# Kernel optimization log

Measured on AMD Instinct MI355X. Metric: run time of the kernel, lower is better.

## Reference

```python
import jax, jax.numpy as jnp
import numpy as np

B, S, H, NH = 2, 2048, 2048, 16
HD = H // NH


def setup_inputs() -> dict:
    key = jax.random.key(0)
    ks = jax.random.split(key, 10)
    s = 1.0 / np.sqrt(H)
    x = jax.random.normal(ks[0], (B, S, H), dtype=jnp.float32)
    # additive causal mask: 0 on/below diagonal, -1e9 above
    causal = jnp.tril(jnp.ones((S, S), dtype=bool))
    mask = jnp.where(causal, 0.0, -1e9).astype(jnp.float32)[None, None]
    return {
        "x": x,
        "mask": mask,
        "wq": jax.random.normal(ks[1], (H, H), jnp.float32) * s,
        "bq": jnp.zeros((H,), jnp.float32),
        "wk": jax.random.normal(ks[2], (H, H), jnp.float32) * s,
        "bk": jnp.zeros((H,), jnp.float32),
        "wv": jax.random.normal(ks[3], (H, H), jnp.float32) * s,
        "bv": jnp.zeros((H,), jnp.float32),
        "wo": jax.random.normal(ks[4], (H, H), jnp.float32) * s,
        "bo": jnp.zeros((H,), jnp.float32),
    }


def reference(x, mask, wq, bq, wk, bk, wv, bv, wo, bo):
    b, s, _ = x.shape
    scale = HD ** (-0.5)
    # projections -> [b, nh, s, hd]
    def split_heads(t):
        return t.reshape(b, s, NH, HD).transpose(0, 2, 1, 3)
    q = split_heads(x @ wq + bq)
    k = split_heads(x @ wk + bk)
    v = split_heads(x @ wv + bv)
    scores = jnp.einsum('bhqd,bhkd->bhqk', q, k) * scale + mask
    attn = jax.nn.softmax(scores, axis=-1)
    out = jnp.einsum('bhqk,bhkd->bhqd', attn, v)
    out = out.transpose(0, 2, 1, 3).reshape(b, s, H)
    return out @ wo + bo
```

## Files before the change

kernel.cpp:

```cpp
#include <hip/hip_runtime.h>


using bf16x8 = __attribute__((ext_vector_type(8))) short;
using bf16x4 = __attribute__((ext_vector_type(4))) short;
using f32x4  = __attribute__((ext_vector_type(4))) float;

#define S_LEN 2048
#define NHEAD 16
#define HDIM  128
#define HID   2048

__device__ __forceinline__ unsigned short f2bf(float f) {
    unsigned int u = __float_as_uint(f);
    u += 0x7fffu + ((u >> 16) & 1u);
    return (unsigned short)(u >> 16);
}
__device__ __forceinline__ void gl2lds16(const void* g, void* l) {
    __builtin_amdgcn_global_load_lds(
        (const __attribute__((address_space(1))) void*)g,
        (__attribute__((address_space(3))) void*)l, 16, 0, 0);
}

__device__ __forceinline__ f32x4 pv_mfma(bf16x4 a, bf16x4 b, f32x4 c) {
#if defined(__HIP_DEVICE_COMPILE__)
#if __has_builtin(__builtin_amdgcn_mfma_f32_16x16x16bf16_1k)
    return __builtin_amdgcn_mfma_f32_16x16x16bf16_1k(a, b, c, 0, 0, 0);
#else
    asm("v_mfma_f32_16x16x16_bf16 %0, %1, %2, %0" : "+v"(c) : "v"(a), "v"(b));
    return c;
#endif
#else
    (void)a; (void)b;
    return c;
#endif
}

__global__ void convert_x(const float* __restrict__ x, unsigned short* __restrict__ xb) {
    int i = (blockIdx.x * 256 + threadIdx.x) * 4;
    float4 v = *(const float4*)(x + i);
    ushort4 o;
    o.x = f2bf(v.x); o.y = f2bf(v.y); o.z = f2bf(v.z); o.w = f2bf(v.w);
    *(ushort4*)(xb + i) = o;
}

__global__ void convert_wt(const float* __restrict__ w0, const float* __restrict__ w1,
                           const float* __restrict__ w2, const float* __restrict__ w3,
                           unsigned short* __restrict__ t0, unsigned short* __restrict__ t1,
                           unsigned short* __restrict__ t2, unsigned short* __restrict__ t3) {
    __shared__ float tile[64][65];
    int z = blockIdx.z;
    const float* src = (z == 0) ? w0 : (z == 1) ? w1 : (z == 2) ? w2 : w3;
    unsigned short* dst = (z == 0) ? t0 : (z == 1) ? t1 : (z == 2) ? t2 : t3;
    int r0 = blockIdx.y * 64, c0 = blockIdx.x * 64;
    int t = threadIdx.x;
    for (int i = t; i < 64 * 64; i += 256) {
        int r = i >> 6, c = i & 63;
        tile[r][c] = src[(size_t)(r0 + r) * HID + c0 + c];
    }
    __syncthreads();
    for (int i = t; i < 64 * 64; i += 256) {
        int r = i & 63, c = i >> 6;
        dst[(size_t)(c0 + c) * HID + r0 + r] = f2bf(tile[r][c]);
    }
}

template <int MODE>
__launch_bounds__(256, 2)
__global__ void gemm_bt(const unsigned short* __restrict__ A,
                        const unsigned short* __restrict__ Bt0,
                        const unsigned short* __restrict__ Bt1,
                        const unsigned short* __restrict__ Bt2,
                        const float* __restrict__ bias0,
                        const float* __restrict__ bias1,
                        const float* __restrict__ bias2,
                        unsigned short* __restrict__ C0,
                        unsigned short* __restrict__ C1,
                        unsigned short* __restrict__ C2,
                        float* __restrict__ Cf) {
    __shared__ __align__(16) unsigned short As[128 * 32];
    __shared__ __align__(16) unsigned short Bs[128 * 32];

    const unsigned short* Bt = Bt0;
    const float* bias = bias0;
    unsigned short* C = C0;
    if (MODE == 1) {
        int z = blockIdx.z;
        if (z == 1) { Bt = Bt1; bias = bias1; C = C1; }
        else if (z == 2) { Bt = Bt2; bias = bias2; C = C2; }
    }

    const int K = HID;
    int m0 = blockIdx.y * 128;
    int n0 = blockIdx.x * 128;
    int tid = threadIdx.x;
    int lane = tid & 63;
    int w = tid >> 6;
    int wr = w >> 1, wc = w & 1;
    int l15 = lane & 15;
    int quad = lane >> 4;

    f32x4 acc[4][4];
#pragma unroll
    for (int i = 0; i < 4; ++i)
#pragma unroll
        for (int j = 0; j < 4; ++j) acc[i][j] = (f32x4){0.f, 0.f, 0.f, 0.f};

    int srow = w * 16 + (lane >> 2);
    int scol = (lane & 3) * 8;
    const unsigned short* gA = A + (size_t)(m0 + srow) * K + scol;
    const unsigned short* gB = Bt + (size_t)(n0 + srow) * K + scol;
    unsigned short* lA = &As[w * 512];
    unsigned short* lB = &Bs[w * 512];

    for (int k0 = 0; k0 < K; k0 += 32) {
        gl2lds16(gA + k0,                  lA);
        gl2lds16(gA + (size_t)64 * K + k0, lA + 2048);
        gl2lds16(gB + k0,                  lB);
        gl2lds16(gB + (size_t)64 * K + k0, lB + 2048);
        __syncthreads();

        bf16x8 av[4], bv[4];
        int q8 = quad * 8;
#pragma unroll
        for (int i = 0; i < 4; ++i) av[i] = *(const bf16x8*)&As[(wr * 64 + i * 16 + l15) * 32 + q8];
#pragma unroll
        for (int j = 0; j < 4; ++j) bv[j] = *(const bf16x8*)&Bs[(wc * 64 + j * 16 + l15) * 32 + q8];
#pragma unroll
        for (int i = 0; i < 4; ++i)
#pragma unroll
            for (int j = 0; j < 4; ++j)
                acc[i][j] = __builtin_amdgcn_mfma_f32_16x16x32_bf16(av[i], bv[j], acc[i][j], 0, 0, 0);
        __syncthreads();
    }

    int zz = (MODE == 1) ? blockIdx.z : 0;
#pragma unroll
    for (int j = 0; j < 4; ++j) {
        int n = n0 + wc * 64 + j * 16 + l15;
        float bn = bias[n];
#pragma unroll
        for (int i = 0; i < 4; ++i) {
            int mb = m0 + wr * 64 + i * 16 + quad * 4;
            if (MODE == 1 && zz == 2) {
                int b = mb >> 11, s = mb & 2047, h = n >> 7, d = n & 127;
                int kt = s >> 4, qv = (s >> 2) & 3, ct = d >> 4, lv = d & 15;
                size_t addr = ((((size_t)((b << 4) + h) * 128 + kt) * 4 + (ct >> 1)) * 4 + qv) * 128
                              + lv * 8 + (ct & 1) * 4;
                ushort4 o;
                o.x = f2bf(acc[i][j][0] + bn);
                o.y = f2bf(acc[i][j][1] + bn);
                o.z = f2bf(acc[i][j][2] + bn);
                o.w = f2bf(acc[i][j][3] + bn);
                *(ushort4*)&C[addr] = o;
            } else {
#pragma unroll
                for (int reg = 0; reg < 4; ++reg) {
                    int m = mb + reg;
                    float v = acc[i][j][reg] + bn;
                    if (MODE == 0) {
                        Cf[(size_t)m * HID + n] = v;
                    } else {
                        int b = m >> 11, s = m & 2047, h = n >> 7, d = n & 127;
                        if (zz == 1) {
                            int kt = s >> 4, lk = s & 15, kk = d >> 5, qk = (d >> 3) & 3, e = d & 7;
                            size_t addr = ((((size_t)((b << 4) + h) * 128 + kt) * 4 + kk) * 4 + qk) * 128
                                          + lk * 8 + e;
                            C[addr] = f2bf(v);
                        } else {
                            C[(size_t)(((b << 4) + h) * S_LEN + s) * HDIM + d] = f2bf(v);
                        }
                    }
                }
            }
        }
    }
}

__launch_bounds__(256, 4)
__global__ void attn_kernel(const unsigned short* __restrict__ Qg,
                            const unsigned short* __restrict__ Kp,
                            const unsigned short* __restrict__ Vp,
                            unsigned short* __restrict__ O) {
    int linear = blockIdx.y * 32 + blockIdx.x;
    int xcd = linear & 7;
    int u = linear >> 3;
    int bh = xcd * 4 + (u & 3);
    int j = u >> 2;
    int b = bh >> 4, h = bh & 15;

    int tid = threadIdx.x, lane = tid & 63, w = tid >> 6;
    int l15 = lane & 15, quad = lane >> 4;

    int role = (w + (u >> 5)) & 3;
    int strip = (role < 2) ? (2 * j + role) : (126 - 2 * j + (role - 2));
    int r0 = strip * 16;

    const unsigned short* Qb = Qg + (size_t)bh * (S_LEN * HDIM);
    const unsigned short* Kb = Kp + (size_t)bh * 262144 + quad * 128 + l15 * 8;
    const unsigned short* Vb = Vp + (size_t)bh * 262144 + quad * 128 + l15 * 8;

    bf16x8 qf[4];
#pragma unroll
    for (int kk = 0; kk < 4; ++kk)
        qf[kk] = *(const bf16x8*)&Qb[(size_t)(r0 + l15) * HDIM + kk * 32 + quad * 8];

    f32x4 o_acc[8];
#pragma unroll
    for (int c = 0; c < 8; ++c) o_acc[c] = (f32x4){0.f, 0.f, 0.f, 0.f};
    float l_part = 0.f;

    const float k2 = 0.08838834764831845f * 1.4426950408889634f;

    int nkt = strip + 1;

    bf16x8 kA[4], kB[4], v[4];

#define LOADK(dst, t) do { size_t _o = (size_t)(t) * 2048;                         \
    dst[0] = *(const bf16x8*)&Kb[_o];                                              \
    dst[1] = *(const bf16x8*)&Kb[_o + 512];                                        \
    dst[2] = *(const bf16x8*)&Kb[_o + 1024];                                       \
    dst[3] = *(const bf16x8*)&Kb[_o + 1536]; } while (0)

#define LOADV(dst, t) do { size_t _o = (size_t)(t) * 2048;                         \
    dst[0] = *(const bf16x8*)&Vb[_o];                                              \
    dst[1] = *(const bf16x8*)&Vb[_o + 512];                                        \
    dst[2] = *(const bf16x8*)&Vb[_o + 1024];                                       \
    dst[3] = *(const bf16x8*)&Vb[_o + 1536]; } while (0)

#define VLO(x) __builtin_shufflevector(x, x, 0, 1, 2, 3)
#define VHI(x) __builtin_shufflevector(x, x, 4, 5, 6, 7)

#define TILE(kreg, t) do {                                                         \
    f32x4 st0 = (f32x4){0.f, 0.f, 0.f, 0.f};                                       \
    f32x4 st1 = (f32x4){0.f, 0.f, 0.f, 0.f};                                       \
    st0 = __builtin_amdgcn_mfma_f32_16x16x32_bf16(kreg[0], qf[0], st0, 0, 0, 0);   \
    st1 = __builtin_amdgcn_mfma_f32_16x16x32_bf16(kreg[1], qf[1], st1, 0, 0, 0);   \
    st0 = __builtin_amdgcn_mfma_f32_16x16x32_bf16(kreg[2], qf[2], st0, 0, 0, 0);   \
    st1 = __builtin_amdgcn_mfma_f32_16x16x32_bf16(kreg[3], qf[3], st1, 0, 0, 0);   \
    f32x4 stv = st0 + st1;                                                         \
    float p0, p1, p2, p3;                                                          \
    if ((t) == nkt - 1) {                                                          \
        p0 = (quad * 4 + 0 <= l15) ? exp2f(stv[0] * k2) : 0.f;                     \
        p1 = (quad * 4 + 1 <= l15) ? exp2f(stv[1] * k2) : 0.f;                     \
        p2 = (quad * 4 + 2 <= l15) ? exp2f(stv[2] * k2) : 0.f;                     \
        p3 = (quad * 4 + 3 <= l15) ? exp2f(stv[3] * k2) : 0.f;                     \
    } else {                                                                       \
        p0 = exp2f(stv[0] * k2); p1 = exp2f(stv[1] * k2);                          \
        p2 = exp2f(stv[2] * k2); p3 = exp2f(stv[3] * k2);                          \
    }                                                                              \
    l_part += (p0 + p1) + (p2 + p3);                                               \
    bf16x4 pf;                                                                     \
    pf[0] = (short)f2bf(p0); pf[1] = (short)f2bf(p1);                              \
    pf[2] = (short)f2bf(p2); pf[3] = (short)f2bf(p3);                              \
    o_acc[0] = pv_mfma(pf, VLO(v[0]), o_acc[0]);                                   \
    o_acc[1] = pv_mfma(pf, VHI(v[0]), o_acc[1]);                                   \
    o_acc[2] = pv_mfma(pf, VLO(v[1]), o_acc[2]);                                   \
    o_acc[3] = pv_mfma(pf, VHI(v[1]), o_acc[3]);                                   \
    o_acc[4] = pv_mfma(pf, VLO(v[2]), o_acc[4]);                                   \
    o_acc[5] = pv_mfma(pf, VHI(v[2]), o_acc[5]);                                   \
    o_acc[6] = pv_mfma(pf, VLO(v[3]), o_acc[6]);                                   \
    o_acc[7] = pv_mfma(pf, VHI(v[3]), o_acc[7]);                                   \
} while (0)

    LOADK(kA, 0);
    int kt = 0;
    while (true) {
        int ktn = (kt + 1 < nkt) ? kt + 1 : kt;
        LOADV(v, kt);
        LOADK(kB, ktn);
        TILE(kA, kt);
        if (++kt >= nkt) break;

        ktn = (kt + 1 < nkt) ? kt + 1 : kt;
        LOADV(v, kt);
        LOADK(kA, ktn);
        TILE(kB, kt);
        if (++kt >= nkt) break;
    }

#undef TILE
#undef LOADK
#undef LOADV
#undef VLO
#undef VHI

    l_part += __shfl_xor(l_part, 16, 64);
    l_part += __shfl_xor(l_part, 32, 64);

#pragma unroll
    for (int reg = 0; reg < 4; ++reg) {
        float l = __shfl(l_part, quad * 4 + reg, 64);
        float inv = 1.f / l;
        int srow = r0 + quad * 4 + reg;
        unsigned short* op = O + (size_t)(b * S_LEN + srow) * HID + h * HDIM;
#pragma unroll
        for (int ct = 0; ct < 8; ++ct)
            op[ct * 16 + l15] = f2bf(o_acc[ct][reg] * inv);
    }
}

extern "C" void kernel_launch(void* const* d_in, const int* in_sizes, int n_in,
                              void* d_out, int out_size, void* d_ws, size_t ws_size,
                              hipStream_t stream) {
    (void)in_sizes; (void)n_in; (void)out_size; (void)ws_size;
    const float* x  = (const float*)d_in[0];
    const float* wq = (const float*)d_in[2];
    const float* bq = (const float*)d_in[3];
    const float* wk = (const float*)d_in[4];
    const float* bk = (const float*)d_in[5];
    const float* wv = (const float*)d_in[6];
    const float* bv = (const float*)d_in[7];
    const float* wo = (const float*)d_in[8];
    const float* bo = (const float*)d_in[9];
    float* out = (float*)d_out;

    unsigned short* ws = (unsigned short*)d_ws;
    const size_t WSZ = 4194304;
    unsigned short* wqT = ws;
    unsigned short* wkT = ws + WSZ;
    unsigned short* wvT = ws + 2 * WSZ;
    unsigned short* woT = ws + 3 * WSZ;
    unsigned short* xb  = ws + 4 * WSZ;
    unsigned short* Ab  = ws + 4 * WSZ;
    unsigned short* Qb  = ws + 6 * WSZ;
    unsigned short* Kb  = ws + 8 * WSZ;
    unsigned short* Vb  = ws + 10 * WSZ;

    convert_x<<<dim3(8192), 256, 0, stream>>>(x, xb);
    convert_wt<<<dim3(32, 32, 4), 256, 0, stream>>>(wq, wk, wv, wo, wqT, wkT, wvT, woT);
    gemm_bt<1><<<dim3(16, 32, 3), 256, 0, stream>>>(xb, wqT, wkT, wvT, bq, bk, bv,
                                                    Qb, Kb, Vb, nullptr);
    attn_kernel<<<dim3(32, 32), 256, 0, stream>>>(Qb, Kb, Vb, Ab);
    gemm_bt<0><<<dim3(16, 32, 1), 256, 0, stream>>>(Ab, woT, nullptr, nullptr,
                                                    bo, nullptr, nullptr,
                                                    nullptr, nullptr, nullptr, out);
}
```

Measured before the change: 424.9 us.

## Rewrite projection GEMMs as 8-wave double-buffered 128x256 tiles with swizzled LDS

Replaces the single-buffered 128x128, 4-wave GEMM with a 512-thread kernel that computes 128x256 tiles over a K=64 step. It double-buffers LDS so global-to-LDS loads overlap MFMA work, using explicit vmcnt/lgkmcnt waits, barriers and setprio. It also XOR-swizzles the LDS layout to avoid bank conflicts and remaps the 1D grid so blocks sharing a weight panel are spread across XCDs. The aim is to hide memory latency and raise MFMA utilisation in the QKV and output projections, at the cost of more LDS (96KB) and hand-tuned synchronisation that is fragile to get right.

```diff
diff --git a/kernel.cpp b/kernel.cpp
--- a/kernel.cpp
+++ b/kernel.cpp
@@ -65,39 +65,56 @@
 }
 
 template <int MODE>
-__launch_bounds__(256, 2)
-__global__ void gemm_bt(const unsigned short* __restrict__ A,
-                        const unsigned short* __restrict__ Bt0,
-                        const unsigned short* __restrict__ Bt1,
-                        const unsigned short* __restrict__ Bt2,
-                        const float* __restrict__ bias0,
-                        const float* __restrict__ bias1,
-                        const float* __restrict__ bias2,
-                        unsigned short* __restrict__ C0,
-                        unsigned short* __restrict__ C1,
-                        unsigned short* __restrict__ C2,
-                        float* __restrict__ Cf) {
-    __shared__ __align__(16) unsigned short As[128 * 32];
-    __shared__ __align__(16) unsigned short Bs[128 * 32];
+__launch_bounds__(512, 2)
+__global__ void gemm8(const unsigned short* __restrict__ A,
+                      const unsigned short* __restrict__ Bt0,
+                      const unsigned short* __restrict__ Bt1,
+                      const unsigned short* __restrict__ Bt2,
+                      const float* __restrict__ bias0,
+                      const float* __restrict__ bias1,
+                      const float* __restrict__ bias2,
+                      unsigned short* __restrict__ C0,
+                      unsigned short* __restrict__ C1,
+                      unsigned short* __restrict__ C2,
+                      float* __restrict__ Cf) {
+    __shared__ __align__(16) unsigned short lds[49152];
+    unsigned short* const A0 = lds;
+    unsigned short* const A1 = lds + 8192;
+    unsigned short* const B0 = lds + 16384;
+    unsigned short* const B1 = lds + 32768;
+
+    const int CPX = (MODE == 1) ? 96 : 32;
+    int vb = (blockIdx.x & 7) * CPX + (blockIdx.x >> 3);
+    int m0  = (vb & 31) * 128;
+    int n0g = (vb >> 5) * 256;
 
     const unsigned short* Bt = Bt0;
     const float* bias = bias0;
     unsigned short* C = C0;
+    int z = 0;
     if (MODE == 1) {
-        int z = blockIdx.z;
+        z = n0g >> 11;
         if (z == 1) { Bt = Bt1; bias = bias1; C = C1; }
         else if (z == 2) { Bt = Bt2; bias = bias2; C = C2; }
     }
-
-    const int K = HID;
-    int m0 = blockIdx.y * 128;
-    int n0 = blockIdx.x * 128;
+    int nb0 = n0g & 2047;
+
     int tid = threadIdx.x;
     int lane = tid & 63;
-    int w = tid >> 6;
-    int wr = w >> 1, wc = w & 1;
-    int l15 = lane & 15;
-    int quad = lane >> 4;
+    int wv_ = tid >> 6;
+    int wr = wv_ >> 2, wc = wv_ & 3;
+    int l15 = lane & 15, quad = lane >> 4;
+
+    int tr = tid >> 3;
+    int tc = ((tid & 7) ^ (tr & 7)) << 3;
+    const unsigned short* gA = A  + (size_t)(m0  + tr) * HID + tc;
+    const unsigned short* gB = Bt + (size_t)(nb0 + tr) * HID + tc;
+    const int td8 = tid * 8;
+
+    int arow = (wr * 64 + l15) * 64;
+    int brow = (wc * 64 + l15) * 64;
+    int sw0 = ((quad ^ (l15 & 7)) << 3);
+    int sw1 = (((4 + quad) ^ (l15 & 7)) << 3);
 
     f32x4 acc[4][4];
 #pragma unroll
@@ -105,43 +122,93 @@
 #pragma unroll
         for (int j = 0; j < 4; ++j) acc[i][j] = (f32x4){0.f, 0.f, 0.f, 0.f};
 
-    int srow = w * 16 + (lane >> 2);
-    int scol = (lane & 3) * 8;
-    const unsigned short* gA = A + (size_t)(m0 + srow) * K + scol;
-    const unsigned short* gB = Bt + (size_t)(n0 + srow) * K + scol;
-    unsigned short* lA = &As[w * 512];
-    unsigned short* lB = &Bs[w * 512];
-
-    for (int k0 = 0; k0 < K; k0 += 32) {
-        gl2lds16(gA + k0,                  lA);
-        gl2lds16(gA + (size_t)64 * K + k0, lA + 2048);
-        gl2lds16(gB + k0,                  lB);
-        gl2lds16(gB + (size_t)64 * K + k0, lB + 2048);
-        __syncthreads();
-
-        bf16x8 av[4], bv[4];
-        int q8 = quad * 8;
-#pragma unroll
-        for (int i = 0; i < 4; ++i) av[i] = *(const bf16x8*)&As[(wr * 64 + i * 16 + l15) * 32 + q8];
-#pragma unroll
-        for (int j = 0; j < 4; ++j) bv[j] = *(const bf16x8*)&Bs[(wc * 64 + j * 16 + l15) * 32 + q8];
-#pragma unroll
-        for (int i = 0; i < 4; ++i)
-#pragma unroll
-            for (int j = 0; j < 4; ++j)
-                acc[i][j] = __builtin_amdgcn_mfma_f32_16x16x32_bf16(av[i], bv[j], acc[i][j], 0, 0, 0);
-        __syncthreads();
-    }
-
-    int zz = (MODE == 1) ? blockIdx.z : 0;
+#define STAGE8(kt, AD, BD) do { int _kc = (kt) * 64;                        \
+    gl2lds16(gA + _kc,              (AD) + td8);                            \
+    gl2lds16(gA + 64 * HID + _kc,   (AD) + 4096 + td8);                     \
+    gl2lds16(gB + _kc,              (BD) + td8);                            \
+    gl2lds16(gB + 64 * HID + _kc,   (BD) + 4096 + td8);                     \
+    gl2lds16(gB + 128 * HID + _kc,  (BD) + 8192 + td8);                     \
+    gl2lds16(gB + 192 * HID + _kc,  (BD) + 12288 + td8); } while (0)
+
+#define FENCE() asm volatile("" ::: "memory")
+#define BAR()   do { FENCE(); __builtin_amdgcn_s_barrier(); FENCE(); } while (0)
+#define WAIT_LGKM0() do { asm volatile("s_waitcnt lgkmcnt(0)" ::: "memory");      \
+                          __builtin_amdgcn_sched_barrier(0); } while (0)
+#define WAIT_VM6()   do { asm volatile("s_waitcnt vmcnt(6)" ::: "memory");        \
+                          __builtin_amdgcn_sched_barrier(0); } while (0)
+
+    auto ktile = [&](unsigned short* AD, unsigned short* BD, int ks) {
+        {
+            bf16x8 av[4], bv[4];
+            av[0] = *(const bf16x8*)(AD + arow + sw0);
+            av[1] = *(const bf16x8*)(AD + arow + 1024 + sw0);
+            av[2] = *(const bf16x8*)(AD + arow + 2048 + sw0);
+            av[3] = *(const bf16x8*)(AD + arow + 3072 + sw0);
+            bv[0] = *(const bf16x8*)(BD + brow + sw0);
+            bv[1] = *(const bf16x8*)(BD + brow + 1024 + sw0);
+            bv[2] = *(const bf16x8*)(BD + brow + 2048 + sw0);
+            bv[3] = *(const bf16x8*)(BD + brow + 3072 + sw0);
+            BAR();
+            WAIT_LGKM0();
+            __builtin_amdgcn_s_setprio(1);
+#pragma unroll
+            for (int mi = 0; mi < 4; ++mi)
+#pragma unroll
+                for (int jj = 0; jj < 4; ++jj)
+                    acc[mi][jj] = __builtin_amdgcn_mfma_f32_16x16x32_bf16(av[mi], bv[jj], acc[mi][jj], 0, 0, 0);
+            __builtin_amdgcn_s_setprio(0);
+            BAR();
+        }
+        {
+            bf16x8 av[4], bv[4];
+            av[0] = *(const bf16x8*)(AD + arow + sw1);
+            av[1] = *(const bf16x8*)(AD + arow + 1024 + sw1);
+            av[2] = *(const bf16x8*)(AD + arow + 2048 + sw1);
+            av[3] = *(const bf16x8*)(AD + arow + 3072 + sw1);
+            bv[0] = *(const bf16x8*)(BD + brow + sw1);
+            bv[1] = *(const bf16x8*)(BD + brow + 1024 + sw1);
+            bv[2] = *(const bf16x8*)(BD + brow + 2048 + sw1);
+            bv[3] = *(const bf16x8*)(BD + brow + 3072 + sw1);
+            WAIT_LGKM0();
+            BAR();
+            STAGE8(ks, AD, BD);
+            __builtin_amdgcn_s_setprio(1);
+#pragma unroll
+            for (int mi = 0; mi < 4; ++mi)
+#pragma unroll
+                for (int jj = 0; jj < 4; ++jj)
+                    acc[mi][jj] = __builtin_amdgcn_mfma_f32_16x16x32_bf16(av[mi], bv[jj], acc[mi][jj], 0, 0, 0);
+            __builtin_amdgcn_s_setprio(0);
+            WAIT_VM6();
+            BAR();
+        }
+    };
+
+    STAGE8(0, A0, B0);
+    STAGE8(1, A1, B1);
+    WAIT_VM6();
+    BAR();
+
+    for (int t = 0; t < 32; t += 2) {
+        ktile(A0, B0, (t + 2 < 32) ? t + 2 : 31);
+        ktile(A1, B1, (t + 3 < 32) ? t + 3 : 31);
+    }
+    asm volatile("s_waitcnt vmcnt(0)" ::: "memory");
+
+#undef STAGE8
+#undef FENCE
+#undef BAR
+#undef WAIT_LGKM0
+#undef WAIT_VM6
+
 #pragma unroll
     for (int j = 0; j < 4; ++j) {
-        int n = n0 + wc * 64 + j * 16 + l15;
+        int n = nb0 + wc * 64 + j * 16 + l15;
         float bn = bias[n];
 #pragma unroll
         for (int i = 0; i < 4; ++i) {
             int mb = m0 + wr * 64 + i * 16 + quad * 4;
-            if (MODE == 1 && zz == 2) {
+            if (MODE == 1 && z == 2) {
                 int b = mb >> 11, s = mb & 2047, h = n >> 7, d = n & 127;
                 int kt = s >> 4, qv = (s >> 2) & 3, ct = d >> 4, lv = d & 15;
                 size_t addr = ((((size_t)((b << 4) + h) * 128 + kt) * 4 + (ct >> 1)) * 4 + qv) * 128
@@ -161,7 +228,7 @@
                         Cf[(size_t)m * HID + n] = v;
                     } else {
                         int b = m >> 11, s = m & 2047, h = n >> 7, d = n & 127;
-                        if (zz == 1) {
+                        if (z == 1) {
                             int kt = s >> 4, lk = s & 15, kk = d >> 5, qk = (d >> 3) & 3, e = d & 7;
                             size_t addr = ((((size_t)((b << 4) + h) * 128 + kt) * 4 + kk) * 4 + qk) * 128
                                           + lk * 8 + e;
@@ -328,10 +395,10 @@
 
     convert_x<<<dim3(8192), 256, 0, stream>>>(x, xb);
     convert_wt<<<dim3(32, 32, 4), 256, 0, stream>>>(wq, wk, wv, wo, wqT, wkT, wvT, woT);
-    gemm_bt<1><<<dim3(16, 32, 3), 256, 0, stream>>>(xb, wqT, wkT, wvT, bq, bk, bv,
-                                                    Qb, Kb, Vb, nullptr);
+    gemm8<1><<<dim3(768), 512, 0, stream>>>(xb, wqT, wkT, wvT, bq, bk, bv,
+                                            Qb, Kb, Vb, nullptr);
     attn_kernel<<<dim3(32, 32), 256, 0, stream>>>(Qb, Kb, Vb, Ab);
-    gemm_bt<0><<<dim3(16, 32, 1), 256, 0, stream>>>(Ab, woT, nullptr, nullptr,
-                                                    bo, nullptr, nullptr,
-                                                    nullptr, nullptr, nullptr, out);
-}
+    gemm8<0><<<dim3(256), 512, 0, stream>>>(Ab, woT, nullptr, nullptr,
+                                            bo, nullptr, nullptr,
+                                            nullptr, nullptr, nullptr, out);
+}
```

Result: faster. 408.9 us (-3.8%).

## Rewrite projection GEMMs as 256x256 double-buffered swizzled MFMA kernel

Applied to the files above, without the earlier changes.

Replaces the 128x128 single-buffered GEMM with a 256x256-tile, 512-thread kernel that uses a K-step of 64. Global-to-LDS loads are double-buffered and interleaved with MFMA work through explicit waitcnt and sched barriers, and the kernel raises wave priority around the MFMA blocks. LDS addresses are XOR-swizzled to avoid bank conflicts, and block IDs are remapped across XCDs. The aim is more data reuse per tile and load latency hidden behind compute. In exchange it uses 128KB of LDS and many more registers per block, and leaves fewer blocks in the grid (128 for the output projection), which may underfill the CUs.

```diff
diff --git a/kernel.cpp b/kernel.cpp
--- a/kernel.cpp
+++ b/kernel.cpp
@@ -65,8 +65,8 @@
 }
 
 template <int MODE>
-__launch_bounds__(256, 2)
-__global__ void gemm_bt(const unsigned short* __restrict__ A,
+__launch_bounds__(512, 2)
+__global__ void gemm256(const unsigned short* __restrict__ A,
                         const unsigned short* __restrict__ Bt0,
                         const unsigned short* __restrict__ Bt1,
                         const unsigned short* __restrict__ Bt2,
@@ -77,71 +77,146 @@
                         unsigned short* __restrict__ C1,
                         unsigned short* __restrict__ C2,
                         float* __restrict__ Cf) {
-    __shared__ __align__(16) unsigned short As[128 * 32];
-    __shared__ __align__(16) unsigned short Bs[128 * 32];
+    __shared__ __align__(16) unsigned short lds[65536];
+    unsigned short* const A0 = lds;
+    unsigned short* const A1 = lds + 16384;
+    unsigned short* const B0 = lds + 32768;
+    unsigned short* const B1 = lds + 49152;
+
+    const int CPX = (MODE == 1) ? 48 : 16;
+    int vb = (blockIdx.x & 7) * CPX + (blockIdx.x >> 3);
+    int m0  = (vb & 15) * 256;
+    int n0g = (vb >> 4) * 256;
 
     const unsigned short* Bt = Bt0;
     const float* bias = bias0;
     unsigned short* C = C0;
+    int z = 0;
     if (MODE == 1) {
-        int z = blockIdx.z;
+        z = n0g >> 11;
         if (z == 1) { Bt = Bt1; bias = bias1; C = C1; }
         else if (z == 2) { Bt = Bt2; bias = bias2; C = C2; }
     }
-
-    const int K = HID;
-    int m0 = blockIdx.y * 128;
-    int n0 = blockIdx.x * 128;
+    int nb0 = n0g & 2047;
+
     int tid = threadIdx.x;
     int lane = tid & 63;
-    int w = tid >> 6;
-    int wr = w >> 1, wc = w & 1;
-    int l15 = lane & 15;
-    int quad = lane >> 4;
-
-    f32x4 acc[4][4];
-#pragma unroll
-    for (int i = 0; i < 4; ++i)
+    int wv_ = tid >> 6;
+    int wr = wv_ >> 2, wc = wv_ & 3;
+    int l15 = lane & 15, quad = lane >> 4;
+
+    int tr = tid >> 3;
+    int tc = ((tid & 7) ^ (tr & 7)) << 3;
+    const unsigned short* gA = A  + (size_t)(m0  + tr) * HID + tc;
+    const unsigned short* gB = Bt + (size_t)(nb0 + tr) * HID + tc;
+    const int td8 = tid * 8;
+
+    int arow0 = (wr * 128 + l15) * 64;
+    int brow0 = (wc * 64 + l15) * 64;
+    int sw0 = ((quad ^ (l15 & 7)) << 3);
+    int sw1 = (((4 + quad) ^ (l15 & 7)) << 3);
+
+    f32x4 acc[8][4];
+#pragma unroll
+    for (int i = 0; i < 8; ++i)
 #pragma unroll
         for (int j = 0; j < 4; ++j) acc[i][j] = (f32x4){0.f, 0.f, 0.f, 0.f};
 
-    int srow = w * 16 + (lane >> 2);
-    int scol = (lane & 3) * 8;
-    const unsigned short* gA = A + (size_t)(m0 + srow) * K + scol;
-    const unsigned short* gB = Bt + (size_t)(n0 + srow) * K + scol;
-    unsigned short* lA = &As[w * 512];
-    unsigned short* lB = &Bs[w * 512];
-
-    for (int k0 = 0; k0 < K; k0 += 32) {
-        gl2lds16(gA + k0,                  lA);
-        gl2lds16(gA + (size_t)64 * K + k0, lA + 2048);
-        gl2lds16(gB + k0,                  lB);
-        gl2lds16(gB + (size_t)64 * K + k0, lB + 2048);
-        __syncthreads();
-
-        bf16x8 av[4], bv[4];
-        int q8 = quad * 8;
-#pragma unroll
-        for (int i = 0; i < 4; ++i) av[i] = *(const bf16x8*)&As[(wr * 64 + i * 16 + l15) * 32 + q8];
-#pragma unroll
-        for (int j = 0; j < 4; ++j) bv[j] = *(const bf16x8*)&Bs[(wc * 64 + j * 16 + l15) * 32 + q8];
-#pragma unroll
-        for (int i = 0; i < 4; ++i)
-#pragma unroll
-            for (int j = 0; j < 4; ++j)
-                acc[i][j] = __builtin_amdgcn_mfma_f32_16x16x32_bf16(av[i], bv[j], acc[i][j], 0, 0, 0);
-        __syncthreads();
-    }
-
-    int zz = (MODE == 1) ? blockIdx.z : 0;
+    bf16x8 aX[4], aY[4], b0v[4], b1v[4];
+
+#define STAGE(kt, AD, BD) do { int _kc = (kt) * 64;                          \
+    gl2lds16(gA + _kc,             (AD) + td8);                              \
+    gl2lds16(gA + 64 * HID + _kc,  (AD) + 4096 + td8);                       \
+    gl2lds16(gA + 128 * HID + _kc, (AD) + 8192 + td8);                       \
+    gl2lds16(gA + 192 * HID + _kc, (AD) + 12288 + td8);                      \
+    gl2lds16(gB + _kc,             (BD) + td8);                              \
+    gl2lds16(gB + 64 * HID + _kc,  (BD) + 4096 + td8);                       \
+    gl2lds16(gB + 128 * HID + _kc, (BD) + 8192 + td8);                       \
+    gl2lds16(gB + 192 * HID + _kc, (BD) + 12288 + td8); } while (0)
+
+#define LDA4(dst, AD, QB, SW) do {                                           \
+    dst[0] = *(const bf16x8*)((AD) + arow0 + ((QB) + 0) * 1024 + (SW));      \
+    dst[1] = *(const bf16x8*)((AD) + arow0 + ((QB) + 1) * 1024 + (SW));      \
+    dst[2] = *(const bf16x8*)((AD) + arow0 + ((QB) + 2) * 1024 + (SW));      \
+    dst[3] = *(const bf16x8*)((AD) + arow0 + ((QB) + 3) * 1024 + (SW)); } while (0)
+
+#define LDB4(dst, BD, SW) do {                                               \
+    dst[0] = *(const bf16x8*)((BD) + brow0 + 0 * 1024 + (SW));               \
+    dst[1] = *(const bf16x8*)((BD) + brow0 + 1 * 1024 + (SW));               \
+    dst[2] = *(const bf16x8*)((BD) + brow0 + 2 * 1024 + (SW));               \
+    dst[3] = *(const bf16x8*)((BD) + brow0 + 3 * 1024 + (SW)); } while (0)
+
+#define MF16(Q, a, b) do {                                                   \
+    __builtin_amdgcn_s_setprio(1);                                           \
+    _Pragma("unroll")                                                        \
+    for (int mi = 0; mi < 4; ++mi)                                           \
+        _Pragma("unroll")                                                    \
+        for (int nj = 0; nj < 4; ++nj)                                       \
+            acc[(Q) * 4 + mi][nj] =                                          \
+                __builtin_amdgcn_mfma_f32_16x16x32_bf16(a[mi], b[nj],        \
+                                                        acc[(Q) * 4 + mi][nj], 0, 0, 0); \
+    __builtin_amdgcn_s_setprio(0); } while (0)
+
+#define SCHED0() __builtin_amdgcn_sched_barrier(0)
+#define BAR()    do { asm volatile("" ::: "memory");                         \
+                      __builtin_amdgcn_s_barrier();                          \
+                      asm volatile("" ::: "memory"); } while (0)
+#define W_LGKM(N) do { asm volatile("s_waitcnt lgkmcnt(" #N ")" ::: "memory"); SCHED0(); } while (0)
+#define W_VM8()   do { asm volatile("s_waitcnt vmcnt(8)" ::: "memory");        SCHED0(); } while (0)
+
+#define TILE4(AD, BD, AN, BN_, ks) do {                                      \
+    LDA4(aY, AD, 4, sw0);                         \
+    W_LGKM(4);                                             \
+    MF16(0, aX, b0v);                                                        \
+    LDA4(aX, AD, 0, sw1);                                                    \
+    LDB4(b1v, BD, sw1);                                \
+    W_LGKM(8);                                                 \
+    MF16(1, aY, b0v);                                                        \
+    LDA4(aY, AD, 4, sw1);                         \
+    W_LGKM(4);                                             \
+    MF16(0, aX, b1v);                                                        \
+    W_LGKM(0);                       \
+    BAR();                               \
+    STAGE(ks, AD, BD);                           \
+    W_VM8();                              \
+    BAR();                                   \
+    LDA4(aX, AN, 0, sw0);                                                    \
+    LDB4(b0v, BN_, sw0);                   \
+    SCHED0();                                                                \
+    MF16(1, aY, b1v);                        \
+} while (0)
+
+    STAGE(0, A0, B0);
+    STAGE(1, A1, B1);
+    W_VM8();
+    BAR();
+    LDA4(aX, A0, 0, sw0);
+    LDB4(b0v, B0, sw0);
+
+    for (int t = 0; t < 32; t += 2) {
+        TILE4(A0, B0, A1, B1, (t + 2 < 32) ? t + 2 : 31);
+        TILE4(A1, B1, A0, B0, (t + 3 < 32) ? t + 3 : 31);
+    }
+    asm volatile("s_waitcnt vmcnt(0) lgkmcnt(0)" ::: "memory");
+
+#undef TILE4
+#undef STAGE
+#undef LDA4
+#undef LDB4
+#undef MF16
+#undef SCHED0
+#undef BAR
+#undef W_LGKM
+#undef W_VM8
+
 #pragma unroll
     for (int j = 0; j < 4; ++j) {
-        int n = n0 + wc * 64 + j * 16 + l15;
+        int n = nb0 + wc * 64 + j * 16 + l15;
         float bn = bias[n];
 #pragma unroll
-        for (int i = 0; i < 4; ++i) {
-            int mb = m0 + wr * 64 + i * 16 + quad * 4;
-            if (MODE == 1 && zz == 2) {
+        for (int i = 0; i < 8; ++i) {
+            int mb = m0 + wr * 128 + i * 16 + quad * 4;
+            if (MODE == 1 && z == 2) {
                 int b = mb >> 11, s = mb & 2047, h = n >> 7, d = n & 127;
                 int kt = s >> 4, qv = (s >> 2) & 3, ct = d >> 4, lv = d & 15;
                 size_t addr = ((((size_t)((b << 4) + h) * 128 + kt) * 4 + (ct >> 1)) * 4 + qv) * 128
@@ -161,7 +236,7 @@
                         Cf[(size_t)m * HID + n] = v;
                     } else {
                         int b = m >> 11, s = m & 2047, h = n >> 7, d = n & 127;
-                        if (zz == 1) {
+                        if (z == 1) {
                             int kt = s >> 4, lk = s & 15, kk = d >> 5, qk = (d >> 3) & 3, e = d & 7;
                             size_t addr = ((((size_t)((b << 4) + h) * 128 + kt) * 4 + kk) * 4 + qk) * 128
                                           + lk * 8 + e;
@@ -328,10 +403,10 @@
 
     convert_x<<<dim3(8192), 256, 0, stream>>>(x, xb);
     convert_wt<<<dim3(32, 32, 4), 256, 0, stream>>>(wq, wk, wv, wo, wqT, wkT, wvT, woT);
-    gemm_bt<1><<<dim3(16, 32, 3), 256, 0, stream>>>(xb, wqT, wkT, wvT, bq, bk, bv,
-                                                    Qb, Kb, Vb, nullptr);
+    gemm256<1><<<dim3(384), 512, 0, stream>>>(xb, wqT, wkT, wvT, bq, bk, bv,
+                                              Qb, Kb, Vb, nullptr);
     attn_kernel<<<dim3(32, 32), 256, 0, stream>>>(Qb, Kb, Vb, Ab);
-    gemm_bt<0><<<dim3(16, 32, 1), 256, 0, stream>>>(Ab, woT, nullptr, nullptr,
-                                                    bo, nullptr, nullptr,
-                                                    nullptr, nullptr, nullptr, out);
-}
+    gemm256<0><<<dim3(128), 512, 0, stream>>>(Ab, woT, nullptr, nullptr,
+                                              bo, nullptr, nullptr,
+                                              nullptr, nullptr, nullptr, out);
+}
```

Measured after the change: 436.5 us. 2.7% more time.
